# Performance work log

Measured on AMD Instinct MI355X. Metric: run time of the kernel, lower is better.

Reference implementation:

```python
import jax, jax.numpy as jnp
import numpy as np

EPS = 1e-7  # keras.backend.epsilon()
ROUTING_ITERS = 3

def squash(v, axis=-1):
    s2 = jnp.sum(jnp.square(v), axis=axis, keepdims=True)
    scale = s2 / (1.0 + s2) / jnp.sqrt(s2 + EPS)
    return scale * v

def setup_inputs() -> dict:
    key = jax.random.key(0)
    k1, k2 = jax.random.split(key)
    B, N_IN, D_IN = 128, 648, 16
    N_OUT, D_OUT = 32, 32
    x = jax.random.normal(k1, (B, N_IN, D_IN), dtype=jnp.float32)
    # glorot-uniform-ish scale for W: shape (N_in, num_caps, cap_dim, d_in)
    limit = np.sqrt(6.0 / (D_IN + D_OUT)).astype(np.float32)
    W = jax.random.uniform(k2, (N_IN, N_OUT, D_OUT, D_IN), dtype=jnp.float32,
                           minval=-limit, maxval=limit)
    return {"x": x, "W": W}

def reference(x, W):
    # prediction vectors u_hat: [B, N_in, N_out, D_out]
    # (original tiles inputs then matmuls W @ u; einsum fuses this)
    u_hat = jnp.einsum('njdi,bni->bnjd', W, x)
    B, N_in, N_out, _ = u_hat.shape
    logits = jnp.zeros((B, N_in, N_out, 1), dtype=u_hat.dtype)
    v = None
    for i in range(ROUTING_ITERS):
        c = jax.nn.softmax(logits, axis=2)                      # [B,N_in,N_out,1]
        s = jnp.sum(c * u_hat, axis=1, keepdims=True)           # [B,1,N_out,D_out]
        v = squash(s, axis=-1)                                  # [B,1,N_out,D_out]
        if i < ROUTING_ITERS - 1:
            agreement = jnp.sum(u_hat * v, axis=-1, keepdims=True)
            logits = logits + agreement
    return jnp.squeeze(v, axis=1)                               # [B,N_out,D_out]
```

## Files before the change

kernel.cpp:

```cpp
#include <hip/hip_runtime.h>
#include <hip/hip_fp16.h>
#include <math.h>


#define N_IN 648
#define ELEMS 131072

#define WF16_OFF 1048576
#define PARTS_OFF 22282240

#define P0X_OFF 131072
#define ARENA_P0 147456

#define XF_OFF 65536
#define LG 69632
#define ARENA_PH 73728

typedef __attribute__((ext_vector_type(8))) _Float16 f16x8;
typedef __attribute__((ext_vector_type(16))) float f32x16;

union F16U { uint4 u; f16x8 f; };
union HU { __half h; unsigned short us; };

__device__ __forceinline__ unsigned pkh(float a, float b) {
  HU x, y; x.h = __float2half(a); y.h = __float2half(b);
  return (unsigned)x.us | ((unsigned)y.us << 16);
}
__device__ __forceinline__ float h2f(unsigned short u) {
  HU x; x.us = u; return __half2float(x.h);
}

__device__ __forceinline__ void writeW(char* wbuf, int jS, int d, const float4* r) {
  uint4 h0, h1;
  h0.x = pkh(r[0].x, r[0].y); h0.y = pkh(r[0].z, r[0].w);
  h0.z = pkh(r[1].x, r[1].y); h0.w = pkh(r[1].z, r[1].w);
  h1.x = pkh(r[2].x, r[2].y); h1.y = pkh(r[2].z, r[2].w);
  h1.z = pkh(r[3].x, r[3].y); h1.w = pkh(r[3].z, r[3].w);
  *(uint4*)(wbuf + jS * 1024 + d * 16) = h0;
  *(uint4*)(wbuf + jS * 1024 + 512 + d * 16) = h1;
}
__device__ __forceinline__ void loadW(float4* r, const float* __restrict__ W,
                                      int n, int jS, int d) {
  const float4* rp = (const float4*)(W + (size_t)n * 16384 + jS * 512 + d * 16);
  r[0] = rp[0]; r[1] = rp[1]; r[2] = rp[2]; r[3] = rp[3];
}

__global__ __launch_bounds__(512) void cvt_w_f16(const float* __restrict__ W,
                                                 char* __restrict__ wf) {
  const int n = blockIdx.x;
  const int t = threadIdx.x;
  const int jS = t >> 4, m = t & 15;
  float4 rA[4], rB[4];
  loadW(rA, W, n, jS, m);
  loadW(rB, W, n, jS, m + 16);
  char* dst = wf + (size_t)n * 32768;
  writeW(dst, jS, m, rA);
  writeW(dst, jS, m + 16, rB);
}

__device__ __forceinline__ void stage_pair(char* nwf, char* nxb,
                                           const char* __restrict__ wf16,
                                           const float* __restrict__ x,
                                           int nbase, int cnt, int b0, int t) {
  const char* src = wf16 + (size_t)nbase * 32768;
  for (int r = 0; r < cnt * 4; ++r)
    *(uint4*)(nwf + r * 8192 + t * 16) = *(const uint4*)(src + r * 8192 + t * 16);
  if (t < 128) {
    const int s2 = t >> 6, u = t & 63;
    if (s2 < cnt) {
      const float4* xp = (const float4*)(
          x + ((size_t)(b0 + (u & 31)) * N_IN + nbase + s2) * 16 + (u >> 5) * 8);
      *(float4*)(nxb + s2 * 2048 + u * 16) = xp[0];
      *(float4*)(nxb + s2 * 2048 + 1024 + u * 16) = xp[1];
    }
  }
}

__device__ __forceinline__ void store_parts(char* arena, __half* __restrict__ parts,
                                            const f32x16* acc, float scale,
                                            int nchunk, int b0, int t) {
  const int w = t >> 6, l = t & 63;
  const int b32 = l & 31, half = l >> 5;
  __syncthreads();
#pragma unroll
  for (int q = 0; q < 4; ++q) {
    const int j = w * 4 + q;
#pragma unroll
    for (int g = 0; g < 4; ++g) {
      float4 v4;
      v4.x = acc[q][g * 4 + 0] * scale;
      v4.y = acc[q][g * 4 + 1] * scale;
      v4.z = acc[q][g * 4 + 2] * scale;
      v4.w = acc[q][g * 4 + 3] * scale;
      *(float4*)(arena + (b32 * 1036 + j * 32 + g * 8 + 4 * half) * 4) = v4;
    }
  }
  __syncthreads();
  char* pb = (char*)(parts + (size_t)nchunk * ELEMS + (size_t)b0 * 1024);
  const int rb = t >> 4, c16 = t & 15;
#pragma unroll
  for (int q = 0; q < 8; ++q) {
    const int g8 = c16 + q * 16;
    const float4 a = *(const float4*)(arena + (rb * 1036 + g8 * 8) * 4);
    const float4 b = *(const float4*)(arena + (rb * 1036 + g8 * 8 + 4) * 4);
    *(uint4*)(pb + rb * 2048 + g8 * 16) =
        uint4{pkh(a.x, a.y), pkh(a.z, a.w), pkh(b.x, b.y), pkh(b.z, b.w)};
  }
}

__device__ __forceinline__ void decode_bid(int bid, int NC, int& nchunk, int& btile) {
  if ((NC & 7) == 0) {
    const int r = bid & 7;
    btile = (bid >> 3) & 3;
    nchunk = (bid >> 5) * 8 + r;
  } else {
    nchunk = bid >> 2;
    btile = bid & 3;
  }
}

__global__ __launch_bounds__(512, 1) void caps_pass0_mfma(
    const float* __restrict__ x, const char* __restrict__ wf16,
    __half* __restrict__ parts, int NC)
{
  __shared__ __align__(16) char arena[ARENA_P0];
  const int t = threadIdx.x;
  const int w = t >> 6, l = t & 63;
  int nchunk, btile;
  decode_bid(blockIdx.x, NC, nchunk, btile);
  const int n0 = (N_IN * nchunk) / NC;
  const int n1 = (N_IN * (nchunk + 1)) / NC;
  const int b0 = btile * 32;

  f32x16 acc[4];
#pragma unroll
  for (int q = 0; q < 4; ++q) acc[q] = (f32x16)(0.0f);

  stage_pair(arena, arena + P0X_OFF, wf16, x, n0, (n1 - n0 >= 2) ? 2 : 1, b0, t);

  int cur = 0;
  for (int base = n0; base < n1; base += 2) {
    const int cnt = (n1 - base >= 2) ? 2 : 1;
    __syncthreads();
    const char* wf = arena + cur * 65536;
    const char* xb = arena + P0X_OFF + cur * 4096;

    for (int s = 0; s < cnt; ++s) {
      const float4 xw0 = *(const float4*)(xb + s * 2048 + l * 16);
      const float4 xw1 = *(const float4*)(xb + s * 2048 + 1024 + l * 16);
      F16U bf;
      bf.u = uint4{pkh(xw0.x, xw0.y), pkh(xw0.z, xw0.w),
                   pkh(xw1.x, xw1.y), pkh(xw1.z, xw1.w)};
#pragma unroll
      for (int q = 0; q < 4; ++q) {
        const int j = w * 4 + q;
        const f16x8 af = *(const f16x8*)(wf + s * 32768 + j * 1024 + l * 16);
        acc[q] = __builtin_amdgcn_mfma_f32_32x32x16_f16(af, bf.f, acc[q], 0, 0, 0);
      }
    }

    if (base + 2 < n1) {
      const int ncnt = (n1 - (base + 2) >= 2) ? 2 : 1;
      stage_pair(arena + (cur ^ 1) * 65536, arena + P0X_OFF + (cur ^ 1) * 4096,
                 wf16, x, base + 2, ncnt, b0, t);
    }
    cur ^= 1;
  }
  store_parts(arena, parts, acc, 0.03125f, nchunk, b0, t);
}

__global__ __launch_bounds__(1024, 1) void caps_phase_mfma(
    const float* __restrict__ x, const char* __restrict__ wf16,
    const float* __restrict__ v,
    __half* __restrict__ parts, int NC)
{
  __shared__ __align__(16) char arena[ARENA_PH];
  const int t = threadIdx.x;
  const int w = t >> 6, l = t & 63;
  const int b32 = l & 31, half = l >> 5;
  int nchunk, btile;
  decode_bid(blockIdx.x, NC, nchunk, btile);
  const int n0 = (N_IN * nchunk) / NC;
  const int n1 = (N_IN * (nchunk + 1)) / NC;
  const int b0 = btile * 32;

  unsigned vw[2][8];
  {
    const int bv = b0 + b32;
#pragma unroll
    for (int q = 0; q < 2; ++q) {
      const int j = w * 2 + q;
#pragma unroll
      for (int g = 0; g < 4; ++g) {
        const float4 g4 = *(const float4*)(v + (size_t)bv * 1024 + j * 32 + g * 8 + 4 * half);
        vw[q][2 * g]     = pkh(g4.x, g4.y);
        vw[q][2 * g + 1] = pkh(g4.z, g4.w);
      }
    }
  }

  {
    const char* src = wf16 + (size_t)n0 * 32768;
    *(uint4*)(arena + t * 16) = *(const uint4*)(src + t * 16);
    *(uint4*)(arena + 16384 + t * 16) = *(const uint4*)(src + 16384 + t * 16);
    if (t < 64) {
      const float4* xp = (const float4*)(x + ((size_t)(b0 + (t & 31)) * N_IN + n0) * 16 + (t >> 5) * 8);
      *(float4*)(arena + XF_OFF + t * 16) = xp[0];
      *(float4*)(arena + XF_OFF + 1024 + t * 16) = xp[1];
    }
  }

  f32x16 acc[2];
  acc[0] = (f32x16)(0.0f);
  acc[1] = (f32x16)(0.0f);

  int cur = 0;
  for (int n = n0; n < n1; ++n) {
    __syncthreads();
    const char* wf = arena + cur * 32768;
    const char* xb = arena + XF_OFF + cur * 2048;
    char* nwf = arena + (cur ^ 1) * 32768;
    char* nxb = arena + XF_OFF + (cur ^ 1) * 2048;
    const bool more = (n + 1 < n1);

    const float4 xw0 = *(const float4*)(xb + l * 16);
    const float4 xw1 = *(const float4*)(xb + 1024 + l * 16);
    F16U bf;
    bf.u = uint4{pkh(xw0.x, xw0.y), pkh(xw0.z, xw0.w),
                 pkh(xw1.x, xw1.y), pkh(xw1.z, xw1.w)};

#pragma unroll
    for (int q = 0; q < 2; ++q) {
      const int j = w * 2 + q;
      const f16x8 af = *(const f16x8*)(wf + j * 1024 + l * 16);
      f32x16 ut = (f32x16)(0.0f);
      ut = __builtin_amdgcn_mfma_f32_32x32x16_f16(af, bf.f, ut, 0, 0, 0);
      float a = 0.f;
#pragma unroll
      for (int k = 0; k < 16; ++k) {
        const unsigned short us = (k & 1) ? (unsigned short)(vw[q][k >> 1] >> 16)
                                          : (unsigned short)(vw[q][k >> 1] & 0xFFFF);
        a = fmaf(ut[k], h2f(us), a);
      }
      a += __shfl_xor(a, 32);
      if (l < 32)
        *(float*)(arena + LG + (j * 32 + ((b32 ^ j) & 31)) * 4) = a;
    }
    __syncthreads();

    {
      const int jj = t & 31, b = (w << 1) | (l >> 5);
      float* slot = (float*)(arena + LG + (jj * 32 + ((b ^ jj) & 31)) * 4);
      float lgv = *slot;
      float mx = lgv;
#pragma unroll
      for (int off = 16; off >= 1; off >>= 1) mx = fmaxf(mx, __shfl_xor(mx, off));
      const float e = __expf(lgv - mx);
      float Z = e;
#pragma unroll
      for (int off = 16; off >= 1; off >>= 1) Z += __shfl_xor(Z, off);
      *slot = e / Z;
    }

    if (more) {
      const char* src = wf16 + (size_t)(n + 1) * 32768;
      *(uint4*)(nwf + t * 16) = *(const uint4*)(src + t * 16);
      *(uint4*)(nwf + 16384 + t * 16) = *(const uint4*)(src + 16384 + t * 16);
      if (t < 64) {
        const float4* xp = (const float4*)(x + ((size_t)(b0 + (t & 31)) * N_IN + n + 1) * 16 + (t >> 5) * 8);
        *(float4*)(nxb + t * 16) = xp[0];
        *(float4*)(nxb + 1024 + t * 16) = xp[1];
      }
    }
    __syncthreads();

#pragma unroll
    for (int q = 0; q < 2; ++q) {
      const int j = w * 2 + q;
      const float cj = *(const float*)(arena + LG + (j * 32 + ((b32 ^ j) & 31)) * 4);
      F16U yf;
      yf.u = uint4{pkh(cj * xw0.x, cj * xw0.y), pkh(cj * xw0.z, cj * xw0.w),
                   pkh(cj * xw1.x, cj * xw1.y), pkh(cj * xw1.z, cj * xw1.w)};
      const f16x8 af = *(const f16x8*)(wf + j * 1024 + l * 16);
      acc[q] = __builtin_amdgcn_mfma_f32_32x32x16_f16(af, yf.f, acc[q], 0, 0, 0);
    }
    cur ^= 1;
  }

#pragma unroll
  for (int r = 0; r < 2; ++r) {
    __syncthreads();
    if ((b32 >> 4) == r) {
      const int b16 = b32 & 15;
#pragma unroll
      for (int q = 0; q < 2; ++q) {
        const int j = w * 2 + q;
#pragma unroll
        for (int g = 0; g < 4; ++g) {
          float4 v4;
          v4.x = acc[q][g * 4 + 0];
          v4.y = acc[q][g * 4 + 1];
          v4.z = acc[q][g * 4 + 2];
          v4.w = acc[q][g * 4 + 3];
          *(float4*)(arena + (b16 * 1036 + j * 32 + g * 8 + 4 * half) * 4) = v4;
        }
      }
    }
    __syncthreads();
    char* pb = (char*)(parts + (size_t)nchunk * ELEMS + (size_t)(b0 + r * 16) * 1024);
    const int rb = t >> 6, c64 = t & 63;
#pragma unroll
    for (int q2 = 0; q2 < 2; ++q2) {
      const int g8 = c64 + q2 * 64;
      const float4 a = *(const float4*)(arena + (rb * 1036 + g8 * 8) * 4);
      const float4 b = *(const float4*)(arena + (rb * 1036 + g8 * 8 + 4) * 4);
      *(uint4*)(pb + rb * 2048 + g8 * 16) =
          uint4{pkh(a.x, a.y), pkh(a.z, a.w), pkh(b.x, b.y), pkh(b.z, b.w)};
    }
  }
}

__global__ void reduce_squash(const unsigned short* __restrict__ parts, int NC,
                              float* __restrict__ out,
                              const float* __restrict__ addprev) {
  const int e = blockIdx.x * 256 + threadIdx.x;
  float s = 0.f;
  for (int c = 0; c < NC; ++c) s += h2f(parts[(size_t)c * ELEMS + e]);
  float s2 = s * s;
#pragma unroll
  for (int off = 16; off >= 1; off >>= 1) s2 += __shfl_xor(s2, off);
  const float scale = (s2 / (1.0f + s2)) * rsqrtf(s2 + 1e-7f);
  const float val = s * scale;
  out[e] = addprev ? (addprev[e] + val) : val;
}

extern "C" void kernel_launch(void* const* d_in, const int* in_sizes, int n_in,
                              void* d_out, int out_size, void* d_ws, size_t ws_size,
                              hipStream_t stream) {
  const float* x = (const float*)d_in[0];
  const float* W = (const float*)d_in[1];
  float* out = (float*)d_out;

  float* v0 = (float*)d_ws;
  float* vsum = v0 + ELEMS;
  char* wf16 = (char*)d_ws + WF16_OFF;
  __half* parts = (__half*)((char*)d_ws + PARTS_OFF);

  size_t rem = ws_size > (size_t)PARTS_OFF ? ws_size - PARTS_OFF : 0;
  int NC = (int)(rem / (ELEMS * 2));
  NC = NC < 1 ? 1 : (NC > 64 ? 64 : NC);

  const dim3 blk(512);
  const dim3 blkP(1024);

  cvt_w_f16<<<dim3(N_IN), blk, 0, stream>>>(W, wf16);

  caps_pass0_mfma<<<dim3(NC * 4), blk, 0, stream>>>(x, wf16, parts, NC);
  reduce_squash<<<512, 256, 0, stream>>>((const unsigned short*)parts, NC, v0, nullptr);

  caps_phase_mfma<<<dim3(NC * 4), blkP, 0, stream>>>(x, wf16, v0, parts, NC);
  reduce_squash<<<512, 256, 0, stream>>>((const unsigned short*)parts, NC, vsum, v0);

  caps_phase_mfma<<<dim3(NC * 4), blkP, 0, stream>>>(x, wf16, vsum, parts, NC);
  reduce_squash<<<512, 256, 0, stream>>>((const unsigned short*)parts, NC, out, nullptr);
}
```

Measured before the change: 141.5 us.

## Reuse u_hat tile for weighted sum, unify pass0 into templated kernel, vectorize reduce

In routing phases the weighted sum is now formed by scaling the already computed u_hat MFMA tile by the coupling coefficient, replacing a second MFMA and the packing of c*x. The separate 512-thread pass-0 kernel is replaced by a ROUTE=0 instantiation of the 1024-thread routing kernel with single-n double buffering. The reduce_squash kernel processes four elements per thread with vector loads and fewer shuffles. The phase loop now keeps u_hat in fp32 registers, which raises register pressure.

```diff
diff --git a/kernel.cpp b/kernel.cpp
--- a/kernel.cpp
+++ b/kernel.cpp
@@ -9,12 +9,9 @@
 #define WF16_OFF 1048576
 #define PARTS_OFF 22282240
 
-#define P0X_OFF 131072
-#define ARENA_P0 147456
-
 #define XF_OFF 65536
 #define LG 69632
-#define ARENA_PH 73728
+#define ARENA 73728
 
 typedef __attribute__((ext_vector_type(8))) _Float16 f16x8;
 typedef __attribute__((ext_vector_type(16))) float f32x16;
@@ -58,56 +55,6 @@
   writeW(dst, jS, m + 16, rB);
 }
 
-__device__ __forceinline__ void stage_pair(char* nwf, char* nxb,
-                                           const char* __restrict__ wf16,
-                                           const float* __restrict__ x,
-                                           int nbase, int cnt, int b0, int t) {
-  const char* src = wf16 + (size_t)nbase * 32768;
-  for (int r = 0; r < cnt * 4; ++r)
-    *(uint4*)(nwf + r * 8192 + t * 16) = *(const uint4*)(src + r * 8192 + t * 16);
-  if (t < 128) {
-    const int s2 = t >> 6, u = t & 63;
-    if (s2 < cnt) {
-      const float4* xp = (const float4*)(
-          x + ((size_t)(b0 + (u & 31)) * N_IN + nbase + s2) * 16 + (u >> 5) * 8);
-      *(float4*)(nxb + s2 * 2048 + u * 16) = xp[0];
-      *(float4*)(nxb + s2 * 2048 + 1024 + u * 16) = xp[1];
-    }
-  }
-}
-
-__device__ __forceinline__ void store_parts(char* arena, __half* __restrict__ parts,
-                                            const f32x16* acc, float scale,
-                                            int nchunk, int b0, int t) {
-  const int w = t >> 6, l = t & 63;
-  const int b32 = l & 31, half = l >> 5;
-  __syncthreads();
-#pragma unroll
-  for (int q = 0; q < 4; ++q) {
-    const int j = w * 4 + q;
-#pragma unroll
-    for (int g = 0; g < 4; ++g) {
-      float4 v4;
-      v4.x = acc[q][g * 4 + 0] * scale;
-      v4.y = acc[q][g * 4 + 1] * scale;
-      v4.z = acc[q][g * 4 + 2] * scale;
-      v4.w = acc[q][g * 4 + 3] * scale;
-      *(float4*)(arena + (b32 * 1036 + j * 32 + g * 8 + 4 * half) * 4) = v4;
-    }
-  }
-  __syncthreads();
-  char* pb = (char*)(parts + (size_t)nchunk * ELEMS + (size_t)b0 * 1024);
-  const int rb = t >> 4, c16 = t & 15;
-#pragma unroll
-  for (int q = 0; q < 8; ++q) {
-    const int g8 = c16 + q * 16;
-    const float4 a = *(const float4*)(arena + (rb * 1036 + g8 * 8) * 4);
-    const float4 b = *(const float4*)(arena + (rb * 1036 + g8 * 8 + 4) * 4);
-    *(uint4*)(pb + rb * 2048 + g8 * 16) =
-        uint4{pkh(a.x, a.y), pkh(a.z, a.w), pkh(b.x, b.y), pkh(b.z, b.w)};
-  }
-}
-
 __device__ __forceinline__ void decode_bid(int bid, int NC, int& nchunk, int& btile) {
   if ((NC & 7) == 0) {
     const int r = bid & 7;
@@ -119,62 +66,13 @@
   }
 }
 
-__global__ __launch_bounds__(512, 1) void caps_pass0_mfma(
-    const float* __restrict__ x, const char* __restrict__ wf16,
-    __half* __restrict__ parts, int NC)
-{
-  __shared__ __align__(16) char arena[ARENA_P0];
-  const int t = threadIdx.x;
-  const int w = t >> 6, l = t & 63;
-  int nchunk, btile;
-  decode_bid(blockIdx.x, NC, nchunk, btile);
-  const int n0 = (N_IN * nchunk) / NC;
-  const int n1 = (N_IN * (nchunk + 1)) / NC;
-  const int b0 = btile * 32;
-
-  f32x16 acc[4];
-#pragma unroll
-  for (int q = 0; q < 4; ++q) acc[q] = (f32x16)(0.0f);
-
-  stage_pair(arena, arena + P0X_OFF, wf16, x, n0, (n1 - n0 >= 2) ? 2 : 1, b0, t);
-
-  int cur = 0;
-  for (int base = n0; base < n1; base += 2) {
-    const int cnt = (n1 - base >= 2) ? 2 : 1;
-    __syncthreads();
-    const char* wf = arena + cur * 65536;
-    const char* xb = arena + P0X_OFF + cur * 4096;
-
-    for (int s = 0; s < cnt; ++s) {
-      const float4 xw0 = *(const float4*)(xb + s * 2048 + l * 16);
-      const float4 xw1 = *(const float4*)(xb + s * 2048 + 1024 + l * 16);
-      F16U bf;
-      bf.u = uint4{pkh(xw0.x, xw0.y), pkh(xw0.z, xw0.w),
-                   pkh(xw1.x, xw1.y), pkh(xw1.z, xw1.w)};
-#pragma unroll
-      for (int q = 0; q < 4; ++q) {
-        const int j = w * 4 + q;
-        const f16x8 af = *(const f16x8*)(wf + s * 32768 + j * 1024 + l * 16);
-        acc[q] = __builtin_amdgcn_mfma_f32_32x32x16_f16(af, bf.f, acc[q], 0, 0, 0);
-      }
-    }
-
-    if (base + 2 < n1) {
-      const int ncnt = (n1 - (base + 2) >= 2) ? 2 : 1;
-      stage_pair(arena + (cur ^ 1) * 65536, arena + P0X_OFF + (cur ^ 1) * 4096,
-                 wf16, x, base + 2, ncnt, b0, t);
-    }
-    cur ^= 1;
-  }
-  store_parts(arena, parts, acc, 0.03125f, nchunk, b0, t);
-}
-
-__global__ __launch_bounds__(1024, 1) void caps_phase_mfma(
+template <int ROUTE>
+__global__ __launch_bounds__(1024, 1) void caps_mfma(
     const float* __restrict__ x, const char* __restrict__ wf16,
     const float* __restrict__ v,
     __half* __restrict__ parts, int NC)
 {
-  __shared__ __align__(16) char arena[ARENA_PH];
+  __shared__ __align__(16) char arena[ARENA];
   const int t = threadIdx.x;
   const int w = t >> 6, l = t & 63;
   const int b32 = l & 31, half = l >> 5;
@@ -185,7 +83,7 @@
   const int b0 = btile * 32;
 
   unsigned vw[2][8];
-  {
+  if (ROUTE) {
     const int bv = b0 + b32;
 #pragma unroll
     for (int q = 0; q < 2; ++q) {
@@ -229,12 +127,34 @@
     bf.u = uint4{pkh(xw0.x, xw0.y), pkh(xw0.z, xw0.w),
                  pkh(xw1.x, xw1.y), pkh(xw1.z, xw1.w)};
 
+    if (ROUTE == 0) {
+#pragma unroll
+      for (int q = 0; q < 2; ++q) {
+        const f16x8 af = *(const f16x8*)(wf + (w * 2 + q) * 1024 + l * 16);
+        acc[q] = __builtin_amdgcn_mfma_f32_32x32x16_f16(af, bf.f, acc[q], 0, 0, 0);
+      }
+      if (more) {
+        const char* src = wf16 + (size_t)(n + 1) * 32768;
+        *(uint4*)(nwf + t * 16) = *(const uint4*)(src + t * 16);
+        *(uint4*)(nwf + 16384 + t * 16) = *(const uint4*)(src + 16384 + t * 16);
+        if (t < 64) {
+          const float4* xp = (const float4*)(x + ((size_t)(b0 + (t & 31)) * N_IN + n + 1) * 16 + (t >> 5) * 8);
+          *(float4*)(nxb + t * 16) = xp[0];
+          *(float4*)(nxb + 1024 + t * 16) = xp[1];
+        }
+      }
+      cur ^= 1;
+      continue;
+    }
+
+    f32x16 u2[2];
 #pragma unroll
     for (int q = 0; q < 2; ++q) {
       const int j = w * 2 + q;
       const f16x8 af = *(const f16x8*)(wf + j * 1024 + l * 16);
       f32x16 ut = (f32x16)(0.0f);
       ut = __builtin_amdgcn_mfma_f32_32x32x16_f16(af, bf.f, ut, 0, 0, 0);
+      u2[q] = ut;
       float a = 0.f;
 #pragma unroll
       for (int k = 0; k < 16; ++k) {
@@ -249,7 +169,7 @@
     __syncthreads();
 
     {
-      const int jj = t & 31, b = (w << 1) | (l >> 5);
+      const int jj = t & 31, b = t >> 5;
       float* slot = (float*)(arena + LG + (jj * 32 + ((b ^ jj) & 31)) * 4);
       float lgv = *slot;
       float mx = lgv;
@@ -278,15 +198,14 @@
     for (int q = 0; q < 2; ++q) {
       const int j = w * 2 + q;
       const float cj = *(const float*)(arena + LG + (j * 32 + ((b32 ^ j) & 31)) * 4);
-      F16U yf;
-      yf.u = uint4{pkh(cj * xw0.x, cj * xw0.y), pkh(cj * xw0.z, cj * xw0.w),
-                   pkh(cj * xw1.x, cj * xw1.y), pkh(cj * xw1.z, cj * xw1.w)};
-      const f16x8 af = *(const f16x8*)(wf + j * 1024 + l * 16);
-      acc[q] = __builtin_amdgcn_mfma_f32_32x32x16_f16(af, yf.f, acc[q], 0, 0, 0);
+#pragma unroll
+      for (int k = 0; k < 16; ++k)
+        acc[q][k] = fmaf(cj, u2[q][k], acc[q][k]);
     }
     cur ^= 1;
   }
 
+  const float scale = (ROUTE == 0) ? 0.03125f : 1.0f;
 #pragma unroll
   for (int r = 0; r < 2; ++r) {
     __syncthreads();
@@ -298,10 +217,10 @@
 #pragma unroll
         for (int g = 0; g < 4; ++g) {
           float4 v4;
-          v4.x = acc[q][g * 4 + 0];
-          v4.y = acc[q][g * 4 + 1];
-          v4.z = acc[q][g * 4 + 2];
-          v4.w = acc[q][g * 4 + 3];
+          v4.x = acc[q][g * 4 + 0] * scale;
+          v4.y = acc[q][g * 4 + 1] * scale;
+          v4.z = acc[q][g * 4 + 2] * scale;
+          v4.w = acc[q][g * 4 + 3] * scale;
           *(float4*)(arena + (b16 * 1036 + j * 32 + g * 8 + 4 * half) * 4) = v4;
         }
       }
@@ -320,18 +239,29 @@
   }
 }
 
-__global__ void reduce_squash(const unsigned short* __restrict__ parts, int NC,
-                              float* __restrict__ out,
-                              const float* __restrict__ addprev) {
-  const int e = blockIdx.x * 256 + threadIdx.x;
-  float s = 0.f;
-  for (int c = 0; c < NC; ++c) s += h2f(parts[(size_t)c * ELEMS + e]);
-  float s2 = s * s;
-#pragma unroll
-  for (int off = 16; off >= 1; off >>= 1) s2 += __shfl_xor(s2, off);
+__global__ void reduce_squash4(const unsigned short* __restrict__ parts, int NC,
+                               float* __restrict__ out,
+                               const float* __restrict__ addprev) {
+  const int e0 = (blockIdx.x * 256 + threadIdx.x) * 4;
+  float s0 = 0.f, s1 = 0.f, s2v = 0.f, s3 = 0.f;
+  for (int c = 0; c < NC; ++c) {
+    const uint2 p = *(const uint2*)(parts + (size_t)c * ELEMS + e0);
+    s0 += h2f((unsigned short)(p.x & 0xFFFF));
+    s1 += h2f((unsigned short)(p.x >> 16));
+    s2v += h2f((unsigned short)(p.y & 0xFFFF));
+    s3 += h2f((unsigned short)(p.y >> 16));
+  }
+  float s2 = s0 * s0 + s1 * s1 + s2v * s2v + s3 * s3;
+#pragma unroll
+  for (int off = 4; off >= 1; off >>= 1) s2 += __shfl_xor(s2, off);
   const float scale = (s2 / (1.0f + s2)) * rsqrtf(s2 + 1e-7f);
-  const float val = s * scale;
-  out[e] = addprev ? (addprev[e] + val) : val;
+  float4 o;
+  o.x = s0 * scale; o.y = s1 * scale; o.z = s2v * scale; o.w = s3 * scale;
+  if (addprev) {
+    const float4 ap = *(const float4*)(addprev + e0);
+    o.x += ap.x; o.y += ap.y; o.z += ap.z; o.w += ap.w;
+  }
+  *(float4*)(out + e0) = o;
 }
 
 extern "C" void kernel_launch(void* const* d_in, const int* in_sizes, int n_in,
@@ -350,17 +280,20 @@
   int NC = (int)(rem / (ELEMS * 2));
   NC = NC < 1 ? 1 : (NC > 64 ? 64 : NC);
 
-  const dim3 blk(512);
-  const dim3 blkP(1024);
-
-  cvt_w_f16<<<dim3(N_IN), blk, 0, stream>>>(W, wf16);
-
-  caps_pass0_mfma<<<dim3(NC * 4), blk, 0, stream>>>(x, wf16, parts, NC);
-  reduce_squash<<<512, 256, 0, stream>>>((const unsigned short*)parts, NC, v0, nullptr);
-
-  caps_phase_mfma<<<dim3(NC * 4), blkP, 0, stream>>>(x, wf16, v0, parts, NC);
-  reduce_squash<<<512, 256, 0, stream>>>((const unsigned short*)parts, NC, vsum, v0);
-
-  caps_phase_mfma<<<dim3(NC * 4), blkP, 0, stream>>>(x, wf16, vsum, parts, NC);
-  reduce_squash<<<512, 256, 0, stream>>>((const unsigned short*)parts, NC, out, nullptr);
-}
+  const dim3 blk512(512);
+  const dim3 blk1k(1024);
+  const dim3 gridP(NC * 4);
+  const dim3 gridR(128);
+  const dim3 blkR(256);
+
+  cvt_w_f16<<<dim3(N_IN), blk512, 0, stream>>>(W, wf16);
+
+  caps_mfma<0><<<gridP, blk1k, 0, stream>>>(x, wf16, nullptr, parts, NC);
+  reduce_squash4<<<gridR, blkR, 0, stream>>>((const unsigned short*)parts, NC, v0, nullptr);
+
+  caps_mfma<1><<<gridP, blk1k, 0, stream>>>(x, wf16, v0, parts, NC);
+  reduce_squash4<<<gridR, blkR, 0, stream>>>((const unsigned short*)parts, NC, vsum, v0);
+
+  caps_mfma<1><<<gridP, blk1k, 0, stream>>>(x, wf16, vsum, parts, NC);
+  reduce_squash4<<<gridR, blkR, 0, stream>>>((const unsigned short*)parts, NC, out, nullptr);
+}
```

Result: slower. 147.5 us (+4.2%).

## Reuse u_hat MFMA output for weighted sum, drop max-softmax and extra barrier

Applied to the files above, without the earlier changes.

The phase kernel now keeps the u_hat MFMA result in registers and accumulates c*u_hat with FMAs instead of issuing a second MFMA on rescaled inputs. Softmax drops the max subtraction and uses a shared-memory atomic sum of exponentials per batch, double-buffered so one barrier per input capsule is removed. Next-tile global loads are issued early into registers to overlap with compute. The reduce/squash kernel is vectorized to four elements per thread. The risk is exp overflow without max subtraction when logits grow large.

```diff
diff --git a/kernel.cpp b/kernel.cpp
--- a/kernel.cpp
+++ b/kernel.cpp
@@ -13,8 +13,8 @@
 #define ARENA_P0 147456
 
 #define XF_OFF 65536
-#define LG 69632
-#define ARENA_PH 73728
+#define ZOFF 69632
+#define ARENA_PH 69888
 
 typedef __attribute__((ext_vector_type(8))) _Float16 f16x8;
 typedef __attribute__((ext_vector_type(16))) float f32x16;
@@ -207,6 +207,7 @@
       const float4* xp = (const float4*)(x + ((size_t)(b0 + (t & 31)) * N_IN + n0) * 16 + (t >> 5) * 8);
       *(float4*)(arena + XF_OFF + t * 16) = xp[0];
       *(float4*)(arena + XF_OFF + 1024 + t * 16) = xp[1];
+      *(float*)(arena + ZOFF + t * 4) = 0.f;
     }
   }
 
@@ -223,18 +224,33 @@
     char* nxb = arena + XF_OFF + (cur ^ 1) * 2048;
     const bool more = (n + 1 < n1);
 
+    uint4 tw0, tw1;
+    float4 xt0, xt1;
+    if (more) {
+      const char* src = wf16 + (size_t)(n + 1) * 32768;
+      tw0 = *(const uint4*)(src + t * 16);
+      tw1 = *(const uint4*)(src + 16384 + t * 16);
+      if (t < 64) {
+        const float4* xp = (const float4*)(x + ((size_t)(b0 + (t & 31)) * N_IN + n + 1) * 16 + (t >> 5) * 8);
+        xt0 = xp[0]; xt1 = xp[1];
+      }
+    }
+
     const float4 xw0 = *(const float4*)(xb + l * 16);
     const float4 xw1 = *(const float4*)(xb + 1024 + l * 16);
     F16U bf;
     bf.u = uint4{pkh(xw0.x, xw0.y), pkh(xw0.z, xw0.w),
                  pkh(xw1.x, xw1.y), pkh(xw1.z, xw1.w)};
 
+    f32x16 u2[2];
+    float e2[2];
 #pragma unroll
     for (int q = 0; q < 2; ++q) {
       const int j = w * 2 + q;
       const f16x8 af = *(const f16x8*)(wf + j * 1024 + l * 16);
       f32x16 ut = (f32x16)(0.0f);
       ut = __builtin_amdgcn_mfma_f32_32x32x16_f16(af, bf.f, ut, 0, 0, 0);
+      u2[q] = ut;
       float a = 0.f;
 #pragma unroll
       for (int k = 0; k < 16; ++k) {
@@ -243,46 +259,33 @@
         a = fmaf(ut[k], h2f(us), a);
       }
       a += __shfl_xor(a, 32);
-      if (l < 32)
-        *(float*)(arena + LG + (j * 32 + ((b32 ^ j) & 31)) * 4) = a;
-    }
-    __syncthreads();
-
-    {
-      const int jj = t & 31, b = (w << 1) | (l >> 5);
-      float* slot = (float*)(arena + LG + (jj * 32 + ((b ^ jj) & 31)) * 4);
-      float lgv = *slot;
-      float mx = lgv;
-#pragma unroll
-      for (int off = 16; off >= 1; off >>= 1) mx = fmaxf(mx, __shfl_xor(mx, off));
-      const float e = __expf(lgv - mx);
-      float Z = e;
-#pragma unroll
-      for (int off = 16; off >= 1; off >>= 1) Z += __shfl_xor(Z, off);
-      *slot = e / Z;
-    }
+      e2[q] = __expf(a);
+    }
+    if (half == 0) {
+      float* Zp = (float*)(arena + ZOFF + cur * 128 + b32 * 4);
+      atomicAdd(Zp, e2[0]);
+      atomicAdd(Zp, e2[1]);
+    }
+    __syncthreads();
 
     if (more) {
-      const char* src = wf16 + (size_t)(n + 1) * 32768;
-      *(uint4*)(nwf + t * 16) = *(const uint4*)(src + t * 16);
-      *(uint4*)(nwf + 16384 + t * 16) = *(const uint4*)(src + 16384 + t * 16);
+      *(uint4*)(nwf + t * 16) = tw0;
+      *(uint4*)(nwf + 16384 + t * 16) = tw1;
       if (t < 64) {
-        const float4* xp = (const float4*)(x + ((size_t)(b0 + (t & 31)) * N_IN + n + 1) * 16 + (t >> 5) * 8);
-        *(float4*)(nxb + t * 16) = xp[0];
-        *(float4*)(nxb + 1024 + t * 16) = xp[1];
-      }
-    }
-    __syncthreads();
-
+        *(float4*)(nxb + t * 16) = xt0;
+        *(float4*)(nxb + 1024 + t * 16) = xt1;
+      }
+    }
+    if (t < 32) *(float*)(arena + ZOFF + (cur ^ 1) * 128 + t * 4) = 0.f;
+
+    const float Zb = *(const float*)(arena + ZOFF + cur * 128 + b32 * 4);
+    const float rZ = __frcp_rn(Zb);
 #pragma unroll
     for (int q = 0; q < 2; ++q) {
-      const int j = w * 2 + q;
-      const float cj = *(const float*)(arena + LG + (j * 32 + ((b32 ^ j) & 31)) * 4);
-      F16U yf;
-      yf.u = uint4{pkh(cj * xw0.x, cj * xw0.y), pkh(cj * xw0.z, cj * xw0.w),
-                   pkh(cj * xw1.x, cj * xw1.y), pkh(cj * xw1.z, cj * xw1.w)};
-      const f16x8 af = *(const f16x8*)(wf + j * 1024 + l * 16);
-      acc[q] = __builtin_amdgcn_mfma_f32_32x32x16_f16(af, yf.f, acc[q], 0, 0, 0);
+      const float cq = e2[q] * rZ;
+#pragma unroll
+      for (int k = 0; k < 16; ++k)
+        acc[q][k] = fmaf(cq, u2[q][k], acc[q][k]);
     }
     cur ^= 1;
   }
@@ -320,18 +323,29 @@
   }
 }
 
-__global__ void reduce_squash(const unsigned short* __restrict__ parts, int NC,
-                              float* __restrict__ out,
-                              const float* __restrict__ addprev) {
-  const int e = blockIdx.x * 256 + threadIdx.x;
-  float s = 0.f;
-  for (int c = 0; c < NC; ++c) s += h2f(parts[(size_t)c * ELEMS + e]);
-  float s2 = s * s;
-#pragma unroll
-  for (int off = 16; off >= 1; off >>= 1) s2 += __shfl_xor(s2, off);
+__global__ void reduce_squash4(const unsigned short* __restrict__ parts, int NC,
+                               float* __restrict__ out,
+                               const float* __restrict__ addprev) {
+  const int e0 = (blockIdx.x * 256 + threadIdx.x) * 4;
+  float s0 = 0.f, s1 = 0.f, s2v = 0.f, s3 = 0.f;
+  for (int c = 0; c < NC; ++c) {
+    const uint2 p = *(const uint2*)(parts + (size_t)c * ELEMS + e0);
+    s0 += h2f((unsigned short)(p.x & 0xFFFF));
+    s1 += h2f((unsigned short)(p.x >> 16));
+    s2v += h2f((unsigned short)(p.y & 0xFFFF));
+    s3 += h2f((unsigned short)(p.y >> 16));
+  }
+  float s2 = s0 * s0 + s1 * s1 + s2v * s2v + s3 * s3;
+#pragma unroll
+  for (int off = 4; off >= 1; off >>= 1) s2 += __shfl_xor(s2, off);
   const float scale = (s2 / (1.0f + s2)) * rsqrtf(s2 + 1e-7f);
-  const float val = s * scale;
-  out[e] = addprev ? (addprev[e] + val) : val;
+  float4 o;
+  o.x = s0 * scale; o.y = s1 * scale; o.z = s2v * scale; o.w = s3 * scale;
+  if (addprev) {
+    const float4 ap = *(const float4*)(addprev + e0);
+    o.x += ap.x; o.y += ap.y; o.z += ap.z; o.w += ap.w;
+  }
+  *(float4*)(out + e0) = o;
 }
 
 extern "C" void kernel_launch(void* const* d_in, const int* in_sizes, int n_in,
@@ -350,17 +364,20 @@
   int NC = (int)(rem / (ELEMS * 2));
   NC = NC < 1 ? 1 : (NC > 64 ? 64 : NC);
 
-  const dim3 blk(512);
-  const dim3 blkP(1024);
-
-  cvt_w_f16<<<dim3(N_IN), blk, 0, stream>>>(W, wf16);
-
-  caps_pass0_mfma<<<dim3(NC * 4), blk, 0, stream>>>(x, wf16, parts, NC);
-  reduce_squash<<<512, 256, 0, stream>>>((const unsigned short*)parts, NC, v0, nullptr);
-
-  caps_phase_mfma<<<dim3(NC * 4), blkP, 0, stream>>>(x, wf16, v0, parts, NC);
-  reduce_squash<<<512, 256, 0, stream>>>((const unsigned short*)parts, NC, vsum, v0);
-
-  caps_phase_mfma<<<dim3(NC * 4), blkP, 0, stream>>>(x, wf16, vsum, parts, NC);
-  reduce_squash<<<512, 256, 0, stream>>>((const unsigned short*)parts, NC, out, nullptr);
-}
+  const dim3 blk512(512);
+  const dim3 blk1k(1024);
+  const dim3 gridP(NC * 4);
+  const dim3 gridR(128);
+  const dim3 blkR(256);
+
+  cvt_w_f16<<<dim3(N_IN), blk512, 0, stream>>>(W, wf16);
+
+  caps_pass0_mfma<<<gridP, blk512, 0, stream>>>(x, wf16, parts, NC);
+  reduce_squash4<<<gridR, blkR, 0, stream>>>((const unsigned short*)parts, NC, v0, nullptr);
+
+  caps_phase_mfma<<<gridP, blk1k, 0, stream>>>(x, wf16, v0, parts, NC);
+  reduce_squash4<<<gridR, blkR, 0, stream>>>((const unsigned short*)parts, NC, vsum, v0);
+
+  caps_phase_mfma<<<gridP, blk1k, 0, stream>>>(x, wf16, vsum, parts, NC);
+  reduce_squash4<<<gridR, blkR, 0, stream>>>((const unsigned short*)parts, NC, out, nullptr);
+}
```

Result: slower. 160.1 us (+13.1%).
